# Kernel optimization log

Measured on AMD Instinct MI355X. Metric: run time of the kernel, lower is better.

## Reference

```python
import jax, jax.numpy as jnp
import numpy as np

ENT_GRID = 16
ENT_DIM = 64
N_RELATION = 5000
EMB_DIM = ENT_GRID * ENT_DIM  # 1024
BATCH = 8192
LN_EPS = 1e-5


def setup_inputs() -> dict:
    key = jax.random.key(0)
    k1, k2, k3, k4 = jax.random.split(key, 4)
    ent_emb = jax.random.normal(k1, (BATCH, EMB_DIM), dtype=jnp.float32)
    proj_ids = jax.random.randint(k2, (BATCH,), 0, N_RELATION, dtype=jnp.int64)
    # xavier_uniform for relation_tran: fan_in = fan_out treated over last two dims
    lim_t = float(np.sqrt(6.0 / (ENT_GRID + ENT_GRID)))
    relation_tran = jax.random.uniform(
        k3, (N_RELATION, ENT_DIM, ENT_GRID, ENT_GRID), jnp.float32, -lim_t, lim_t)
    lim_b = float(np.sqrt(6.0 / (ENT_DIM + ENT_GRID)))
    relation_bias = jax.random.uniform(
        k4, (N_RELATION, ENT_DIM, ENT_GRID), jnp.float32, -lim_b, lim_b)
    ln_weight = jnp.ones((EMB_DIM,), dtype=jnp.float32)
    ln_bias = jnp.zeros((EMB_DIM,), dtype=jnp.float32)
    return {
        "ent_emb": ent_emb,
        "proj_ids": proj_ids,
        "relation_tran": relation_tran,
        "relation_bias": relation_bias,
        "ln_weight": ln_weight,
        "ln_bias": ln_bias,
    }


def _layer_norm(x, w, b, eps=LN_EPS):
    mu = jnp.mean(x, axis=-1, keepdims=True)
    var = jnp.mean(jnp.square(x - mu), axis=-1, keepdims=True)
    return (x - mu) * jax.lax.rsqrt(var + eps) * w + b


def reference(ent_emb, proj_ids, relation_tran, relation_bias, ln_weight, ln_bias):
    B = ent_emb.shape[0]
    # gather per-query relation transform and bias
    rel_tran = relation_tran[proj_ids]  # (B, ent_dim, g, g)
    rel_bias = relation_bias[proj_ids]  # (B, ent_dim, g)
    # distribute: (B, emb_dim) -> (B, ent_dim, ent_grid); torch.chunk+stack == contiguous reshape
    e = ent_emb.reshape(B, ENT_DIM, ENT_GRID)
    # batched small matmul: (g,g) @ (g,) per (batch, ent_dim) block, plus bias
    x = jnp.einsum('bdgh,bdh->bdg', rel_tran, e) + rel_bias
    out = _layer_norm(x.reshape(B, EMB_DIM), ln_weight, ln_bias)
    return out
```

## Files before the change

kernel.cpp:

```cpp
#include <hip/hip_runtime.h>

#define ENT_GRID 16
#define ENT_DIM  64
#define EMB      1024
#define LN_EPS   1e-5f
#define NXCD     8


__global__ void zero_hist_kernel(int* __restrict__ hist, int n) {
    int i = blockIdx.x * blockDim.x + threadIdx.x;
    if (i < n) hist[i] = 0;
}

__global__ void hist_kernel(const int* __restrict__ ids, int* __restrict__ hist, int B) {
    int i = blockIdx.x * blockDim.x + threadIdx.x;
    if (i < B) atomicAdd(&hist[ids[i]], 1);
}

__global__ __launch_bounds__(1024)
void scan_kernel(const int* __restrict__ hist, int* __restrict__ cursor, int n) {
    const int t = threadIdx.x;
    const int ITEMS = (n + 1023) / 1024;
    int vals[8];
    int lsum = 0;
#pragma unroll
    for (int k = 0; k < 8; ++k) {
        int i = t * ITEMS + k;
        int v = (k < ITEMS && i < n) ? hist[i] : 0;
        vals[k] = v;
        lsum += v;
    }
    __shared__ int s[1024];
    s[t] = lsum;
    __syncthreads();
    for (int off = 1; off < 1024; off <<= 1) {
        int v = (t >= off) ? s[t - off] : 0;
        __syncthreads();
        s[t] += v;
        __syncthreads();
    }
    int run = s[t] - lsum;
#pragma unroll
    for (int k = 0; k < 8; ++k) {
        int i = t * ITEMS + k;
        if (k < ITEMS && i < n) cursor[i] = run;
        run += vals[k];
    }
}

__global__ void scatter_kernel(const int* __restrict__ ids, int* __restrict__ cursor,
                               int* __restrict__ perm, int B) {
    int i = blockIdx.x * blockDim.x + threadIdx.x;
    if (i < B) {
        int pos = atomicAdd(&cursor[ids[i]], 1);
        perm[pos] = i;
    }
}

__global__ __launch_bounds__(256, 4)
void wproj_ln_kernel(const float* __restrict__ ent_emb,
                     const float* __restrict__ rel_tran,
                     const float* __restrict__ rel_bias,
                     const float* __restrict__ ln_w,
                     const float* __restrict__ ln_b,
                     const int*   __restrict__ proj_ids,
                     const int*   __restrict__ perm,
                     float* __restrict__ out,
                     int nblk_per_xcd, int use_swizzle) {
    int g = blockIdx.x;
    if (use_swizzle) {
        g = (g % NXCD) * nblk_per_xcd + g / NXCD;
    }
    const int b = perm[g];
    const int t = threadIdx.x;

    const long long r = (long long)proj_ids[b];
    const float* __restrict__ tran = rel_tran + (size_t)r * (ENT_DIM * ENT_GRID * ENT_GRID);
    const float* __restrict__ bias = rel_bias + (size_t)r * (ENT_DIM * ENT_GRID);
    const float* __restrict__ e    = ent_emb  + (size_t)b * EMB;

    __shared__ float se[EMB];
    __shared__ float wsum[4], wsq[4];

    reinterpret_cast<float4*>(se)[t] = reinterpret_cast<const float4*>(e)[t];
    __syncthreads();

    float x[4];
    float sum = 0.0f, sumsq = 0.0f;

#pragma unroll
    for (int k = 0; k < 4; ++k) {
        const int i = t + k * 256;
        const int d = i >> 4;
        const float4* __restrict__ tr = reinterpret_cast<const float4*>(tran + (size_t)i * ENT_GRID);
        const float4* __restrict__ er = reinterpret_cast<const float4*>(se + d * ENT_GRID);
        float acc = bias[i];
#pragma unroll
        for (int q = 0; q < 4; ++q) {
            float4 a  = tr[q];
            float4 ev = er[q];
            acc += a.x * ev.x + a.y * ev.y + a.z * ev.z + a.w * ev.w;
        }
        x[k]  = acc;
        sum   += acc;
        sumsq += acc * acc;
    }

#pragma unroll
    for (int off = 32; off > 0; off >>= 1) {
        sum   += __shfl_xor(sum, off, 64);
        sumsq += __shfl_xor(sumsq, off, 64);
    }
    const int wid = t >> 6;
    if ((t & 63) == 0) { wsum[wid] = sum; wsq[wid] = sumsq; }
    __syncthreads();

    const float tsum = wsum[0] + wsum[1] + wsum[2] + wsum[3];
    const float tsq  = wsq[0]  + wsq[1]  + wsq[2]  + wsq[3];
    const float mu   = tsum * (1.0f / (float)EMB);
    const float var  = tsq * (1.0f / (float)EMB) - mu * mu;
    const float rstd = rsqrtf(var + LN_EPS);

    float* __restrict__ ob = out + (size_t)b * EMB;
#pragma unroll
    for (int k = 0; k < 4; ++k) {
        const int i = t + k * 256;
        ob[i] = (x[k] - mu) * rstd * ln_w[i] + ln_b[i];
    }
}

extern "C" void kernel_launch(void* const* d_in, const int* in_sizes, int n_in,
                              void* d_out, int out_size, void* d_ws, size_t ws_size,
                              hipStream_t stream) {
    const float* ent_emb  = (const float*)d_in[0];
    const int*   proj_ids = (const int*)  d_in[1];
    const float* rel_tran = (const float*)d_in[2];
    const float* rel_bias = (const float*)d_in[3];
    const float* ln_w     = (const float*)d_in[4];
    const float* ln_b     = (const float*)d_in[5];
    float* out = (float*)d_out;

    const int B  = in_sizes[1];
    const int NR = in_sizes[2] / (ENT_DIM * ENT_GRID * ENT_GRID);

    int* w      = (int*)d_ws;
    int* hist   = w;
    int* cursor = w + NR;
    int* perm   = w + 2 * NR;

    zero_hist_kernel<<<(NR + 255) / 256, 256, 0, stream>>>(hist, NR);
    hist_kernel<<<(B + 255) / 256, 256, 0, stream>>>(proj_ids, hist, B);
    scan_kernel<<<1, 1024, 0, stream>>>(hist, cursor, NR);
    scatter_kernel<<<(B + 255) / 256, 256, 0, stream>>>(proj_ids, cursor, perm, B);

    const int use_swizzle = (B % NXCD == 0) ? 1 : 0;
    wproj_ln_kernel<<<B, 256, 0, stream>>>(ent_emb, rel_tran, rel_bias, ln_w, ln_b,
                                           proj_ids, perm, out, B / NXCD, use_swizzle);
}
```

Baseline: 95.74 us.

## Process all queries sharing a relation in one block with registers-cached transform

```diff
diff --git a/kernel.cpp b/kernel.cpp
--- a/kernel.cpp
+++ b/kernel.cpp
@@ -4,7 +4,6 @@
 #define ENT_DIM  64
 #define EMB      1024
 #define LN_EPS   1e-5f
-#define NXCD     8
 
 
 __global__ void zero_hist_kernel(int* __restrict__ hist, int n) {
@@ -58,74 +57,87 @@
 }
 
 __global__ __launch_bounds__(256, 4)
-void wproj_ln_kernel(const float* __restrict__ ent_emb,
-                     const float* __restrict__ rel_tran,
-                     const float* __restrict__ rel_bias,
-                     const float* __restrict__ ln_w,
-                     const float* __restrict__ ln_b,
-                     const int*   __restrict__ proj_ids,
-                     const int*   __restrict__ perm,
-                     float* __restrict__ out,
-                     int nblk_per_xcd, int use_swizzle) {
-    int g = blockIdx.x;
-    if (use_swizzle) {
-        g = (g % NXCD) * nblk_per_xcd + g / NXCD;
-    }
-    const int b = perm[g];
+void wproj_group_kernel(const float* __restrict__ ent_emb,
+                        const float* __restrict__ rel_tran,
+                        const float* __restrict__ rel_bias,
+                        const float* __restrict__ ln_w,
+                        const float* __restrict__ ln_b,
+                        const int*   __restrict__ hist,
+                        const int*   __restrict__ cursor_end,
+                        const int*   __restrict__ perm,
+                        float* __restrict__ out) {
+    const int r   = blockIdx.x;
+    const int cnt = hist[r];
+    if (cnt == 0) return;
+    const int start = cursor_end[r] - cnt;
     const int t = threadIdx.x;
 
-    const long long r = (long long)proj_ids[b];
     const float* __restrict__ tran = rel_tran + (size_t)r * (ENT_DIM * ENT_GRID * ENT_GRID);
     const float* __restrict__ bias = rel_bias + (size_t)r * (ENT_DIM * ENT_GRID);
-    const float* __restrict__ e    = ent_emb  + (size_t)b * EMB;
+
+    float4 trv[4][4];
+    float  bias_v[4], lw[4], lb[4];
+#pragma unroll
+    for (int k = 0; k < 4; ++k) {
+        const int i = t + k * 256;
+        const float4* __restrict__ trp = reinterpret_cast<const float4*>(tran + (size_t)i * ENT_GRID);
+#pragma unroll
+        for (int q = 0; q < 4; ++q) trv[k][q] = trp[q];
+        bias_v[k] = bias[i];
+        lw[k] = ln_w[i];
+        lb[k] = ln_b[i];
+    }
 
     __shared__ float se[EMB];
     __shared__ float wsum[4], wsq[4];
 
-    reinterpret_cast<float4*>(se)[t] = reinterpret_cast<const float4*>(e)[t];
-    __syncthreads();
+    for (int j = 0; j < cnt; ++j) {
+        const int b = perm[start + j];
 
-    float x[4];
-    float sum = 0.0f, sumsq = 0.0f;
+        reinterpret_cast<float4*>(se)[t] =
+            reinterpret_cast<const float4*>(ent_emb + (size_t)b * EMB)[t];
+        __syncthreads();
+
+        float x[4];
+        float sum = 0.0f, sumsq = 0.0f;
+#pragma unroll
+        for (int k = 0; k < 4; ++k) {
+            const int d = (t >> 4) + k * 16;
+            const float4* __restrict__ er = reinterpret_cast<const float4*>(se + d * ENT_GRID);
+            float acc = bias_v[k];
+#pragma unroll
+            for (int q = 0; q < 4; ++q) {
+                float4 a  = trv[k][q];
+                float4 ev = er[q];
+                acc += a.x * ev.x + a.y * ev.y + a.z * ev.z + a.w * ev.w;
+            }
+            x[k]  = acc;
+            sum   += acc;
+            sumsq += acc * acc;
+        }
 
 #pragma unroll
-    for (int k = 0; k < 4; ++k) {
-        const int i = t + k * 256;
-        const int d = i >> 4;
-        const float4* __restrict__ tr = reinterpret_cast<const float4*>(tran + (size_t)i * ENT_GRID);
-        const float4* __restrict__ er = reinterpret_cast<const float4*>(se + d * ENT_GRID);
-        float acc = bias[i];
+        for (int off = 32; off > 0; off >>= 1) {
+            sum   += __shfl_xor(sum, off, 64);
+            sumsq += __shfl_xor(sumsq, off, 64);
+        }
+        const int wid = t >> 6;
+        if ((t & 63) == 0) { wsum[wid] = sum; wsq[wid] = sumsq; }
+        __syncthreads();
+
+        const float tsum = wsum[0] + wsum[1] + wsum[2] + wsum[3];
+        const float tsq  = wsq[0]  + wsq[1]  + wsq[2]  + wsq[3];
+        const float mu   = tsum * (1.0f / (float)EMB);
+        const float var  = tsq * (1.0f / (float)EMB) - mu * mu;
+        const float rstd = rsqrtf(var + LN_EPS);
+
+        float* __restrict__ ob = out + (size_t)b * EMB;
 #pragma unroll
-        for (int q = 0; q < 4; ++q) {
-            float4 a  = tr[q];
-            float4 ev = er[q];
-            acc += a.x * ev.x + a.y * ev.y + a.z * ev.z + a.w * ev.w;
+        for (int k = 0; k < 4; ++k) {
+            const int i = t + k * 256;
+            ob[i] = (x[k] - mu) * rstd * lw[k] + lb[k];
         }
-        x[k]  = acc;
-        sum   += acc;
-        sumsq += acc * acc;
-    }
-
-#pragma unroll
-    for (int off = 32; off > 0; off >>= 1) {
-        sum   += __shfl_xor(sum, off, 64);
-        sumsq += __shfl_xor(sumsq, off, 64);
-    }
-    const int wid = t >> 6;
-    if ((t & 63) == 0) { wsum[wid] = sum; wsq[wid] = sumsq; }
-    __syncthreads();
-
-    const float tsum = wsum[0] + wsum[1] + wsum[2] + wsum[3];
-    const float tsq  = wsq[0]  + wsq[1]  + wsq[2]  + wsq[3];
-    const float mu   = tsum * (1.0f / (float)EMB);
-    const float var  = tsq * (1.0f / (float)EMB) - mu * mu;
-    const float rstd = rsqrtf(var + LN_EPS);
-
-    float* __restrict__ ob = out + (size_t)b * EMB;
-#pragma unroll
-    for (int k = 0; k < 4; ++k) {
-        const int i = t + k * 256;
-        ob[i] = (x[k] - mu) * rstd * ln_w[i] + ln_b[i];
+        __syncthreads();
     }
 }
 
@@ -153,7 +165,6 @@
     scan_kernel<<<1, 1024, 0, stream>>>(hist, cursor, NR);
     scatter_kernel<<<(B + 255) / 256, 256, 0, stream>>>(proj_ids, cursor, perm, B);
 
-    const int use_swizzle = (B % NXCD == 0) ? 1 : 0;
-    wproj_ln_kernel<<<B, 256, 0, stream>>>(ent_emb, rel_tran, rel_bias, ln_w, ln_b,
-                                           proj_ids, perm, out, B / NXCD, use_swizzle);
+    wproj_group_kernel<<<NR, 256, 0, stream>>>(ent_emb, rel_tran, rel_bias, ln_w, ln_b,
+                                               hist, cursor, perm, out);
 }
```

Result: faster. 90.51 us (-5.5%).
